# Performance work log

Measured on AMD Instinct MI355X. Metric: run time of the kernel, lower is better.

The kernel has to match this reference:

```python
import jax, jax.numpy as jnp
import numpy as np

EPS = 1e-8
TEMP = 1.0
NUM_SUPERPIXEL = 2048
NUM_SMALL = 8192  # args.small_nseg


def setup_inputs() -> dict:
    key = jax.random.key(0)
    ks = jax.random.split(key, 9)
    N, C, H, W = 4, 19, 512, 512
    S, Ssm = NUM_SUPERPIXEL, NUM_SMALL
    return {
        "inputs": jax.random.normal(ks[0], (N, C, H, W), jnp.float32),
        "inputs_weak": jax.random.normal(ks[1], (N, C, H, W), jnp.float32),
        "targets": jax.random.bernoulli(ks[2], 0.1, (N, S, C + 1)).astype(jnp.float32),
        "spmasks": jax.random.bernoulli(ks[3], 0.8, (N, H, W)),
        "spmasks_weak": jax.random.bernoulli(ks[4], 0.8, (N, H, W)),
        "superpixels": jax.random.randint(ks[5], (N, H, W), 0, S, jnp.int32),
        "superpixels_weak": jax.random.randint(ks[6], (N, H, W), 0, S, jnp.int32),
        "superpixel_smalls": jax.random.randint(ks[7], (N, H, W), 0, Ssm, jnp.int32),
        "spx_smalls_weak": jax.random.randint(ks[8], (N, H, W), 0, Ssm, jnp.int32),
    }


def _per_sample(out_w, seg_w_raw, mask_w, small_w, trg, nll, seg_s_raw, mask_s):
    # out_w: [HWo, C] weak softmax; nll: [HW, C] strong -log softmax
    HWo, C = out_w.shape
    S, Ssm = NUM_SUPERPIXEL, NUM_SMALL
    # route invalid weak pixels to dummy segment S (mimics boolean compaction)
    seg_w = jnp.where(mask_w, seg_w_raw, S)
    max_v = jax.ops.segment_max(out_w, seg_w, num_segments=S + 1)  # [S+1, C]
    pix = jnp.arange(HWo, dtype=jnp.int32)[:, None]
    cand = jnp.where(out_w == max_v[seg_w], pix, HWo)
    idx = jax.ops.segment_min(cand, seg_w, num_segments=S + 1)[:S]  # [S, C] argmax pixel per (sp, class)
    has_pixel = idx[:, 0] < HWo  # superpixel received >=1 valid pixel (scatter_max OOR filter)
    sel_small = small_w[jnp.clip(idx, 0, HWo - 1)]  # [S, C] small-spx id of per-class argmax pixel
    pair = has_pixel[:, None] & (trg > 0)  # selected (superpixel, class) pairs
    # strong branch: per-small-superpixel NLL sum + pixel counts
    seg_s = jnp.where(mask_s, seg_s_raw, Ssm)
    sumpool = jax.ops.segment_sum(nll, seg_s, num_segments=Ssm + 1)[:Ssm]  # [Ssm, C]
    counts = jax.ops.segment_sum(mask_s.astype(jnp.int32), seg_s, num_segments=Ssm + 1)[:Ssm]  # [Ssm]
    val = sumpool[sel_small, jnp.arange(C)[None, :]]  # [S, C]
    sz = counts[sel_small]  # [S, C]
    loss_i = jnp.sum(jnp.where(pair, val, 0.0))
    nv_i = jnp.sum(jnp.where(pair, sz, 0))
    return loss_i, nv_i


def reference(inputs, inputs_weak, targets, spmasks, spmasks_weak,
              superpixels, superpixels_weak, superpixel_smalls, spx_smalls_weak):
    N, C, H, W = inputs.shape
    out_w = jax.nn.softmax(inputs_weak / TEMP, axis=1).transpose(0, 2, 3, 1).reshape(N, -1, C)
    out_s = jax.nn.softmax(inputs / TEMP, axis=1).transpose(0, 2, 3, 1).reshape(N, -1, C)
    nll = -jnp.log(out_s + EPS)
    loss_i, nv_i = jax.vmap(_per_sample)(
        out_w,
        superpixels_weak.reshape(N, -1),
        spmasks_weak.reshape(N, -1),
        spx_smalls_weak.reshape(N, -1),
        targets[..., :-1],
        nll,
        superpixel_smalls.reshape(N, -1),
        spmasks.reshape(N, -1),
    )
    num_valid = 1 + jnp.sum(nv_i)
    return jnp.sum(loss_i) / num_valid.astype(jnp.float32)
```

## Files before the change

kernel.cpp:

```cpp
#include <hip/hip_runtime.h>

constexpr int kN = 4, kC = 19, kH = 512, kW = 512;
constexpr int kHW = kH * kW;
constexpr int kS = 2048;
constexpr int kSsm = 8192;
constexpr float kEps = 1e-8f;

constexpr int kNSC = kN * kS * kC;
constexpr int kCombineBlocks = 304;

constexpr size_t OFF_AMAX = 0;
constexpr size_t SZ_AMAX  = (size_t)kN * kS * kC * 8;
constexpr size_t OFF_SUM  = OFF_AMAX + SZ_AMAX;
constexpr size_t SZ_SUM   = (size_t)kN * kSsm * kC * 4;
constexpr size_t OFF_CNT  = OFF_SUM + SZ_SUM;
constexpr size_t SZ_CNT   = (size_t)kN * kSsm * 4;
constexpr size_t OFF_NM   = OFF_CNT + SZ_CNT;
constexpr size_t SZ_NM    = (size_t)kN * kSsm * 4;
constexpr size_t ZERO_BYTES = OFF_NM + SZ_NM;
constexpr size_t ZERO_CHUNKS = ZERO_BYTES / 16;
constexpr size_t OFF_TM   = ZERO_BYTES;
constexpr size_t SZ_TM    = (size_t)kN * kS * 4;
constexpr size_t OFF_PL   = OFF_TM + SZ_TM;
constexpr size_t SZ_PL    = (size_t)kCombineBlocks * 4;
constexpr size_t OFF_PN   = OFF_PL + SZ_PL;
constexpr size_t SZ_PN    = (size_t)kCombineBlocks * 4;
constexpr size_t WS_TOTAL = OFF_PN + SZ_PN;

__global__ void init_kernel(const float* __restrict__ targets,
                            unsigned* __restrict__ tmask,
                            ulong2* __restrict__ ws) {
    size_t gid = (size_t)blockIdx.x * blockDim.x + threadIdx.x;
    if (gid < ZERO_CHUNKS) ws[gid] = ulong2{0ULL, 0ULL};
    if (gid < (size_t)kN * kS) {
        const float* t = targets + gid * (kC + 1);
        unsigned m = 0;
#pragma unroll
        for (int c = 0; c < kC; ++c)
            if (t[c] > 0.f) m |= (1u << c);
        tmask[gid] = m;
    }
}

__global__ void weak_argmax_kernel(const float* __restrict__ logits,
                                   const unsigned char* __restrict__ mask,
                                   const int* __restrict__ seg,
                                   const unsigned* __restrict__ tmask,
                                   unsigned long long* __restrict__ amax) {
    int gid = blockIdx.x * blockDim.x + threadIdx.x;
    if (gid >= kN * kHW) return;
    if (!mask[gid]) return;
    int n = gid / kHW;
    int p = gid - n * kHW;
    int s = seg[gid];
    unsigned tm = tmask[n * kS + s];
    if (!tm) return;

    const float* base = logits + (size_t)n * kC * kHW + p;
    float sum = 0.f;
#pragma unroll
    for (int c = 0; c < kC; ++c)
        sum += __expf(base[(size_t)c * kHW]);
    float inv = 1.f / sum;

    unsigned long long lowbits = (unsigned int)(~(unsigned int)p);
    unsigned long long* dst = amax + ((size_t)n * kS + s) * kC;
    unsigned bits = tm;
    while (bits) {
        int c = __ffs(bits) - 1;
        bits &= bits - 1;
        float v = __expf(base[(size_t)c * kHW]) * inv;
        unsigned long long key =
            ((unsigned long long)__float_as_uint(v) << 32) | lowbits;
        atomicMax(&dst[c], key);
    }
}

__global__ void need_mark_kernel(const unsigned long long* __restrict__ amax,
                                 const unsigned* __restrict__ tmask,
                                 const int* __restrict__ small_w,
                                 unsigned* __restrict__ needmask) {
    int gid = blockIdx.x * blockDim.x + threadIdx.x;
    if (gid >= kNSC) return;
    int n = gid / (kS * kC);
    int rem = gid - n * (kS * kC);
    int s = rem / kC;
    int c = rem - s * kC;
    if (!((tmask[n * kS + s] >> c) & 1u)) return;
    unsigned long long packed = amax[gid];
    if (packed == 0ULL) return;
    unsigned pix = ~(unsigned)(packed & 0xFFFFFFFFULL);
    int sel = small_w[(size_t)n * kHW + pix];
    atomicOr(&needmask[n * kSsm + sel], 1u << c);
}

__global__ void strong_sumpool_kernel(const float* __restrict__ logits,
                                      const unsigned char* __restrict__ mask,
                                      const int* __restrict__ seg,
                                      const unsigned* __restrict__ needmask,
                                      float* __restrict__ sumpool,
                                      int* __restrict__ counts) {
    int gid = blockIdx.x * blockDim.x + threadIdx.x;
    if (gid >= kN * kHW) return;
    if (!mask[gid]) return;
    int n = gid / kHW;
    int p = gid - n * kHW;
    int ss = seg[gid];
    unsigned nm = needmask[n * kSsm + ss];
    if (!nm) return;

    const float* base = logits + (size_t)n * kC * kHW + p;
    float sum = 0.f;
#pragma unroll
    for (int c = 0; c < kC; ++c)
        sum += __expf(base[(size_t)c * kHW]);
    float inv = 1.f / sum;

    float* dst = sumpool + ((size_t)n * kSsm + ss) * kC;
    unsigned bits = nm;
    while (bits) {
        int c = __ffs(bits) - 1;
        bits &= bits - 1;
        float v = __expf(base[(size_t)c * kHW]) * inv;
        atomicAdd(&dst[c], -__logf(v + kEps));
    }
    atomicAdd(&counts[n * kSsm + ss], 1);
}

__global__ void combine_kernel(const unsigned long long* __restrict__ amax,
                               const unsigned* __restrict__ tmask,
                               const int* __restrict__ small_w,
                               const float* __restrict__ sumpool,
                               const int* __restrict__ counts,
                               float* __restrict__ ploss,
                               int* __restrict__ pnv) {
    __shared__ float sLoss[8];
    __shared__ int sNv[8];
    int gid = blockIdx.x * blockDim.x + threadIdx.x;
    float lv = 0.f;
    int nvv = 0;
    {
        int n = gid / (kS * kC);
        int rem = gid - n * (kS * kC);
        int s = rem / kC;
        int c = rem - s * kC;
        if ((tmask[n * kS + s] >> c) & 1u) {
            unsigned long long packed = amax[gid];
            if (packed != 0ULL) {
                unsigned pix = ~(unsigned)(packed & 0xFFFFFFFFULL);
                int sel = small_w[(size_t)n * kHW + pix];
                lv = sumpool[((size_t)n * kSsm + sel) * kC + c];
                nvv = counts[n * kSsm + sel];
            }
        }
    }
#pragma unroll
    for (int off = 32; off > 0; off >>= 1) {
        lv += __shfl_down(lv, off);
        nvv += __shfl_down(nvv, off);
    }
    int wave = threadIdx.x >> 6;
    if ((threadIdx.x & 63) == 0) {
        sLoss[wave] = lv;
        sNv[wave] = nvv;
    }
    __syncthreads();
    if (threadIdx.x == 0) {
        float tl = 0.f;
        int tn = 0;
#pragma unroll
        for (int w = 0; w < 8; ++w) {
            tl += sLoss[w];
            tn += sNv[w];
        }
        ploss[blockIdx.x] = tl;
        pnv[blockIdx.x] = tn;
    }
}

__global__ void finalize_kernel(const float* __restrict__ ploss,
                                const int* __restrict__ pnv,
                                float* __restrict__ out) {
    __shared__ float sLoss[4];
    __shared__ int sNv[4];
    float lv = 0.f;
    int nvv = 0;
    for (int i = threadIdx.x; i < kCombineBlocks; i += 256) {
        lv += ploss[i];
        nvv += pnv[i];
    }
#pragma unroll
    for (int off = 32; off > 0; off >>= 1) {
        lv += __shfl_down(lv, off);
        nvv += __shfl_down(nvv, off);
    }
    int wave = threadIdx.x >> 6;
    if ((threadIdx.x & 63) == 0) {
        sLoss[wave] = lv;
        sNv[wave] = nvv;
    }
    __syncthreads();
    if (threadIdx.x == 0) {
        float tl = sLoss[0] + sLoss[1] + sLoss[2] + sLoss[3];
        int tn = sNv[0] + sNv[1] + sNv[2] + sNv[3];
        out[0] = tl / (float)(1 + tn);
    }
}

extern "C" void kernel_launch(void* const* d_in, const int* in_sizes, int n_in,
                              void* d_out, int out_size, void* d_ws, size_t ws_size,
                              hipStream_t stream) {
    const float* inputs            = (const float*)d_in[0];
    const float* inputs_weak       = (const float*)d_in[1];
    const float* targets           = (const float*)d_in[2];
    const unsigned char* spmasks      = (const unsigned char*)d_in[3];
    const unsigned char* spmasks_weak = (const unsigned char*)d_in[4];
    const int* superpixels_weak    = (const int*)d_in[6];
    const int* superpixel_smalls   = (const int*)d_in[7];
    const int* spx_smalls_weak     = (const int*)d_in[8];
    float* out = (float*)d_out;

    unsigned long long* amax = (unsigned long long*)((char*)d_ws + OFF_AMAX);
    float* sumpool           = (float*)((char*)d_ws + OFF_SUM);
    int* counts              = (int*)((char*)d_ws + OFF_CNT);
    unsigned* needmask       = (unsigned*)((char*)d_ws + OFF_NM);
    unsigned* tmask          = (unsigned*)((char*)d_ws + OFF_TM);
    float* ploss             = (float*)((char*)d_ws + OFF_PL);
    int* pnv                 = (int*)((char*)d_ws + OFF_PN);

    int initThreads = (int)ZERO_CHUNKS;
    init_kernel<<<(initThreads + 255) / 256, 256, 0, stream>>>(targets, tmask,
                                                               (ulong2*)d_ws);
    int pixTotal = kN * kHW;
    int pixBlocks = (pixTotal + 255) / 256;
    weak_argmax_kernel<<<pixBlocks, 256, 0, stream>>>(inputs_weak, spmasks_weak,
                                                      superpixels_weak, tmask, amax);
    need_mark_kernel<<<(kNSC + 255) / 256, 256, 0, stream>>>(amax, tmask,
                                                             spx_smalls_weak, needmask);
    strong_sumpool_kernel<<<pixBlocks, 256, 0, stream>>>(inputs, spmasks,
                                                         superpixel_smalls,
                                                         needmask, sumpool, counts);
    combine_kernel<<<kCombineBlocks, 512, 0, stream>>>(amax, tmask, spx_smalls_weak,
                                                       sumpool, counts, ploss, pnv);
    finalize_kernel<<<1, 256, 0, stream>>>(ploss, pnv, out);
}
```

Baseline: 65.23 us.

## Fold combine into strong pass via per-(small,class) multiplicity weights

Instead of accumulating per-small-superpixel NLL sums and counts with atomics and then gathering them in a combine kernel, the need-mark pass now counts how many selected (superpixel, class) pairs point to each (small superpixel, class). The strong pass then weights each pixel's NLL by that multiplicity and reduces directly into per-block partials. This removes the float and int atomics on sumpool and counts as well as one kernel launch. In exchange it adds a multiplicity read per set bit and a finalize that has to sum 4096 partials instead of 304.

```diff
diff --git a/kernel.cpp b/kernel.cpp
--- a/kernel.cpp
+++ b/kernel.cpp
@@ -7,24 +7,22 @@
 constexpr float kEps = 1e-8f;
 
 constexpr int kNSC = kN * kS * kC;
-constexpr int kCombineBlocks = 304;
+constexpr int kPixBlocks = kN * kHW / 256;
 
 constexpr size_t OFF_AMAX = 0;
 constexpr size_t SZ_AMAX  = (size_t)kN * kS * kC * 8;
-constexpr size_t OFF_SUM  = OFF_AMAX + SZ_AMAX;
-constexpr size_t SZ_SUM   = (size_t)kN * kSsm * kC * 4;
-constexpr size_t OFF_CNT  = OFF_SUM + SZ_SUM;
-constexpr size_t SZ_CNT   = (size_t)kN * kSsm * 4;
-constexpr size_t OFF_NM   = OFF_CNT + SZ_CNT;
+constexpr size_t OFF_MULT = OFF_AMAX + SZ_AMAX;
+constexpr size_t SZ_MULT  = (size_t)kN * kSsm * kC * 4;
+constexpr size_t OFF_NM   = OFF_MULT + SZ_MULT;
 constexpr size_t SZ_NM    = (size_t)kN * kSsm * 4;
 constexpr size_t ZERO_BYTES = OFF_NM + SZ_NM;
 constexpr size_t ZERO_CHUNKS = ZERO_BYTES / 16;
 constexpr size_t OFF_TM   = ZERO_BYTES;
 constexpr size_t SZ_TM    = (size_t)kN * kS * 4;
 constexpr size_t OFF_PL   = OFF_TM + SZ_TM;
-constexpr size_t SZ_PL    = (size_t)kCombineBlocks * 4;
+constexpr size_t SZ_PL    = (size_t)kPixBlocks * 4;
 constexpr size_t OFF_PN   = OFF_PL + SZ_PL;
-constexpr size_t SZ_PN    = (size_t)kCombineBlocks * 4;
+constexpr size_t SZ_PN    = (size_t)kPixBlocks * 4;
 constexpr size_t WS_TOTAL = OFF_PN + SZ_PN;
 
 __global__ void init_kernel(const float* __restrict__ targets,
@@ -79,7 +77,8 @@
 __global__ void need_mark_kernel(const unsigned long long* __restrict__ amax,
                                  const unsigned* __restrict__ tmask,
                                  const int* __restrict__ small_w,
-                                 unsigned* __restrict__ needmask) {
+                                 unsigned* __restrict__ needmask,
+                                 unsigned* __restrict__ mult) {
     int gid = blockIdx.x * blockDim.x + threadIdx.x;
     if (gid >= kNSC) return;
     int n = gid / (kS * kC);
@@ -92,89 +91,60 @@
     unsigned pix = ~(unsigned)(packed & 0xFFFFFFFFULL);
     int sel = small_w[(size_t)n * kHW + pix];
     atomicOr(&needmask[n * kSsm + sel], 1u << c);
-}
-
-__global__ void strong_sumpool_kernel(const float* __restrict__ logits,
-                                      const unsigned char* __restrict__ mask,
-                                      const int* __restrict__ seg,
-                                      const unsigned* __restrict__ needmask,
-                                      float* __restrict__ sumpool,
-                                      int* __restrict__ counts) {
+    atomicAdd(&mult[((size_t)n * kSsm + sel) * kC + c], 1u);
+}
+
+__global__ void strong_loss_kernel(const float* __restrict__ logits,
+                                   const unsigned char* __restrict__ mask,
+                                   const int* __restrict__ seg,
+                                   const unsigned* __restrict__ needmask,
+                                   const unsigned* __restrict__ mult,
+                                   float* __restrict__ ploss,
+                                   int* __restrict__ pnv) {
+    __shared__ float sLoss[4];
+    __shared__ int sNv[4];
     int gid = blockIdx.x * blockDim.x + threadIdx.x;
-    if (gid >= kN * kHW) return;
-    if (!mask[gid]) return;
-    int n = gid / kHW;
-    int p = gid - n * kHW;
-    int ss = seg[gid];
-    unsigned nm = needmask[n * kSsm + ss];
-    if (!nm) return;
-
-    const float* base = logits + (size_t)n * kC * kHW + p;
-    float sum = 0.f;
-#pragma unroll
-    for (int c = 0; c < kC; ++c)
-        sum += __expf(base[(size_t)c * kHW]);
-    float inv = 1.f / sum;
-
-    float* dst = sumpool + ((size_t)n * kSsm + ss) * kC;
-    unsigned bits = nm;
-    while (bits) {
-        int c = __ffs(bits) - 1;
-        bits &= bits - 1;
-        float v = __expf(base[(size_t)c * kHW]) * inv;
-        atomicAdd(&dst[c], -__logf(v + kEps));
-    }
-    atomicAdd(&counts[n * kSsm + ss], 1);
-}
-
-__global__ void combine_kernel(const unsigned long long* __restrict__ amax,
-                               const unsigned* __restrict__ tmask,
-                               const int* __restrict__ small_w,
-                               const float* __restrict__ sumpool,
-                               const int* __restrict__ counts,
-                               float* __restrict__ ploss,
-                               int* __restrict__ pnv) {
-    __shared__ float sLoss[8];
-    __shared__ int sNv[8];
-    int gid = blockIdx.x * blockDim.x + threadIdx.x;
-    float lv = 0.f;
+    float loss = 0.f;
     int nvv = 0;
-    {
-        int n = gid / (kS * kC);
-        int rem = gid - n * (kS * kC);
-        int s = rem / kC;
-        int c = rem - s * kC;
-        if ((tmask[n * kS + s] >> c) & 1u) {
-            unsigned long long packed = amax[gid];
-            if (packed != 0ULL) {
-                unsigned pix = ~(unsigned)(packed & 0xFFFFFFFFULL);
-                int sel = small_w[(size_t)n * kHW + pix];
-                lv = sumpool[((size_t)n * kSsm + sel) * kC + c];
-                nvv = counts[n * kSsm + sel];
+    if (mask[gid]) {
+        int n = gid / kHW;
+        int p = gid - n * kHW;
+        int ss = seg[gid];
+        unsigned nm = needmask[n * kSsm + ss];
+        if (nm) {
+            const float* base = logits + (size_t)n * kC * kHW + p;
+            float sum = 0.f;
+#pragma unroll
+            for (int c = 0; c < kC; ++c)
+                sum += __expf(base[(size_t)c * kHW]);
+            float inv = 1.f / sum;
+
+            const unsigned* row = mult + ((size_t)n * kSsm + ss) * kC;
+            unsigned bits = nm;
+            while (bits) {
+                int c = __ffs(bits) - 1;
+                bits &= bits - 1;
+                unsigned m = row[c];
+                float v = __expf(base[(size_t)c * kHW]) * inv;
+                loss += (float)m * (-__logf(v + kEps));
+                nvv += (int)m;
             }
         }
     }
 #pragma unroll
     for (int off = 32; off > 0; off >>= 1) {
-        lv += __shfl_down(lv, off);
+        loss += __shfl_down(loss, off);
         nvv += __shfl_down(nvv, off);
     }
     int wave = threadIdx.x >> 6;
     if ((threadIdx.x & 63) == 0) {
-        sLoss[wave] = lv;
+        sLoss[wave] = loss;
         sNv[wave] = nvv;
     }
     __syncthreads();
     if (threadIdx.x == 0) {
-        float tl = 0.f;
-        int tn = 0;
-#pragma unroll
-        for (int w = 0; w < 8; ++w) {
-            tl += sLoss[w];
-            tn += sNv[w];
-        }
-        ploss[blockIdx.x] = tl;
-        pnv[blockIdx.x] = tn;
+        ploss[blockIdx.x] = sLoss[0] + sLoss[1] + sLoss[2] + sLoss[3];
+        pnv[blockIdx.x]   = sNv[0] + sNv[1] + sNv[2] + sNv[3];
     }
 }
 
@@ -185,7 +155,7 @@
     __shared__ int sNv[4];
     float lv = 0.f;
     int nvv = 0;
-    for (int i = threadIdx.x; i < kCombineBlocks; i += 256) {
+    for (int i = threadIdx.x; i < kPixBlocks; i += 256) {
         lv += ploss[i];
         nvv += pnv[i];
     }
@@ -221,8 +191,7 @@
     float* out = (float*)d_out;
 
     unsigned long long* amax = (unsigned long long*)((char*)d_ws + OFF_AMAX);
-    float* sumpool           = (float*)((char*)d_ws + OFF_SUM);
-    int* counts              = (int*)((char*)d_ws + OFF_CNT);
+    unsigned* mult           = (unsigned*)((char*)d_ws + OFF_MULT);
     unsigned* needmask       = (unsigned*)((char*)d_ws + OFF_NM);
     unsigned* tmask          = (unsigned*)((char*)d_ws + OFF_TM);
     float* ploss             = (float*)((char*)d_ws + OFF_PL);
@@ -231,16 +200,13 @@
     int initThreads = (int)ZERO_CHUNKS;
     init_kernel<<<(initThreads + 255) / 256, 256, 0, stream>>>(targets, tmask,
                                                                (ulong2*)d_ws);
-    int pixTotal = kN * kHW;
-    int pixBlocks = (pixTotal + 255) / 256;
-    weak_argmax_kernel<<<pixBlocks, 256, 0, stream>>>(inputs_weak, spmasks_weak,
-                                                      superpixels_weak, tmask, amax);
+    weak_argmax_kernel<<<kPixBlocks, 256, 0, stream>>>(inputs_weak, spmasks_weak,
+                                                       superpixels_weak, tmask, amax);
     need_mark_kernel<<<(kNSC + 255) / 256, 256, 0, stream>>>(amax, tmask,
-                                                             spx_smalls_weak, needmask);
-    strong_sumpool_kernel<<<pixBlocks, 256, 0, stream>>>(inputs, spmasks,
-                                                         superpixel_smalls,
-                                                         needmask, sumpool, counts);
-    combine_kernel<<<kCombineBlocks, 512, 0, stream>>>(amax, tmask, spx_smalls_weak,
-                                                       sumpool, counts, ploss, pnv);
+                                                             spx_smalls_weak,
+                                                             needmask, mult);
+    strong_loss_kernel<<<kPixBlocks, 256, 0, stream>>>(inputs, spmasks,
+                                                       superpixel_smalls,
+                                                       needmask, mult, ploss, pnv);
     finalize_kernel<<<1, 256, 0, stream>>>(ploss, pnv, out);
 }
```

Measured after the change: 61.43 us. 5.8% less time.
